# Kernel optimization log

Measured on AMD Instinct MI355X. Metric: run time of the kernel, lower is better.

Reference implementation:

```python
import jax, jax.numpy as jnp
import numpy as np

EPS = 1e-5
NH, NP = 12, 4  # heads, points per level


def _ln(x, g, b):
    m = x.mean(-1, keepdims=True)
    v = x.var(-1, keepdims=True)
    return (x - m) / jnp.sqrt(v + EPS) * g + b


def _bilinear(v, g, H_, W_):
    # v: [B, nh, H_*W_, d] flattened feature map; g: [B, nh, Lq, np, 2] normalized locs in [0,1]
    # torch grid_sample(align_corners=False, padding='zeros') with grid = 2*loc-1 => pixel = loc*W - 0.5
    x = g[..., 0] * W_ - 0.5
    y = g[..., 1] * H_ - 0.5
    x0 = jnp.floor(x)
    y0 = jnp.floor(y)
    wx1 = x - x0
    wy1 = y - y0
    wx0 = 1.0 - wx1
    wy0 = 1.0 - wy1
    d = v.shape[-1]
    Bn, nh, Lq, np_ = x.shape
    out = jnp.zeros((Bn, nh, Lq, np_, d), v.dtype)
    for xi, yi, w in ((x0, y0, wx0 * wy0), (x0 + 1, y0, wx1 * wy0),
                      (x0, y0 + 1, wx0 * wy1), (x0 + 1, y0 + 1, wx1 * wy1)):
        valid = (xi >= 0) & (xi < W_) & (yi >= 0) & (yi < H_)
        xc = jnp.clip(xi, 0, W_ - 1).astype(jnp.int32)
        yc = jnp.clip(yi, 0, H_ - 1).astype(jnp.int32)
        idx = (yc * W_ + xc).reshape(Bn, nh, Lq * np_, 1)
        gv = jnp.take_along_axis(v, idx, axis=2).reshape(Bn, nh, Lq, np_, d)
        out = out + (w * valid.astype(v.dtype))[..., None] * gv
    return out


def setup_inputs() -> dict:
    key = jax.random.key(0)
    ks = jax.random.split(key, 16)
    B, Lq, C = 4, 4096, 768
    nl = 1
    Hs = Ws = 64
    Lin = Hs * Ws
    hid = int(C * 0.25)
    s = 0.02
    f32 = jnp.float32
    return {
        'query': jax.random.normal(ks[0], (B, Lq, C), f32),
        'reference_points': jax.random.uniform(ks[1], (B, Lq, nl, 2), f32),
        'feat': jax.random.normal(ks[2], (B, Lin, C), f32),
        'spatial_shapes': np.array([[Hs, Ws]], dtype=np.int64),
        'level_start_index': np.array([0], dtype=np.int64),
        'H': Hs, 'W': Ws,
        'qn_g': jnp.ones(C, f32), 'qn_b': jnp.zeros(C, f32),
        'fn_g': jnp.ones(C, f32), 'fn_b': jnp.zeros(C, f32),
        'Wv': jax.random.normal(ks[3], (C, C), f32) * s, 'bv': jnp.zeros(C, f32),
        'Woff': jax.random.normal(ks[4], (C, NH * nl * NP * 2), f32) * s,
        'boff': jax.random.normal(ks[5], (NH * nl * NP * 2,), f32) * 0.1,
        'Watt': jax.random.normal(ks[6], (C, NH * nl * NP), f32) * s,
        'batt': jnp.zeros(NH * nl * NP, f32),
        'Wout': jax.random.normal(ks[7], (C, C), f32) * s, 'bout': jnp.zeros(C, f32),
        'ffn_g': jnp.ones(C, f32), 'ffn_b': jnp.zeros(C, f32),
        'W1': jax.random.normal(ks[8], (C, hid), f32) * s, 'b1': jnp.zeros(hid, f32),
        'W2': jax.random.normal(ks[9], (hid, C), f32) * s, 'b2': jnp.zeros(C, f32),
    }


def reference(query, reference_points, feat, spatial_shapes, level_start_index, H, W,
              qn_g, qn_b, fn_g, fn_b, Wv, bv, Woff, boff, Watt, batt, Wout, bout,
              ffn_g, ffn_b, W1, b1, W2, b2):
    B, Lq, C = query.shape
    nl = spatial_shapes.shape[0]
    d = C // NH
    qn = _ln(query, qn_g, qn_b)
    fn = _ln(feat, fn_g, fn_b)
    value = (fn @ Wv + bv).reshape(B, -1, NH, d)
    off = (qn @ Woff + boff).reshape(B, Lq, NH, nl, NP, 2)
    attw = jax.nn.softmax((qn @ Watt + batt).reshape(B, Lq, NH, nl * NP), axis=-1)
    attw = attw.reshape(B, Lq, NH, nl, NP)
    # offset normalizer is [W_l, H_l]
    norm = np.stack([spatial_shapes[:, 1], spatial_shapes[:, 0]], -1).astype(np.float32)
    loc = reference_points[:, :, None, :, None, :] + off / jnp.asarray(norm)[None, None, None, :, None, :]
    out = jnp.zeros((B, NH, Lq, d), query.dtype)
    for l in range(nl):
        H_, W_ = int(spatial_shapes[l, 0]), int(spatial_shapes[l, 1])
        s0 = int(level_start_index[l])
        v = value[:, s0:s0 + H_ * W_].transpose(0, 2, 1, 3)       # [B, nh, HW, d]
        g = loc[:, :, :, l].transpose(0, 2, 1, 3, 4)              # [B, nh, Lq, np, 2]
        sampled = _bilinear(v, g, H_, W_)                         # [B, nh, Lq, np, d]
        w = attw[:, :, :, l].transpose(0, 2, 1, 3)                # [B, nh, Lq, np]
        out = out + jnp.sum(sampled * w[..., None], axis=3)
    attn = out.transpose(0, 2, 1, 3).reshape(B, Lq, C) @ Wout + bout
    query = query + attn
    h = _ln(query, ffn_g, ffn_b)
    h = jax.nn.gelu(h @ W1 + b1, approximate=False)
    return query + (h @ W2 + b2)
```

## Files before the change

### kernel.cpp

```cpp
#include <hip/hip_runtime.h>
#include <hip/hip_bf16.h>
#include <math.h>

#define B_    4
#define LQ    4096
#define CC    768
#define NH_   12
#define DH    64
#define NP_   4
#define HH    64
#define WW    64
#define HID   192
#define ROWS  (B_ * LQ)
#define EPS_  1e-5f

typedef __bf16 bf16x8 __attribute__((ext_vector_type(8)));
typedef __bf16 bf16x4 __attribute__((ext_vector_type(4)));
typedef float  f32x4  __attribute__((ext_vector_type(4)));

typedef __attribute__((address_space(3))) void* lds_vp;
typedef const __attribute__((address_space(1))) void* gbl_vp;

struct PrepJob { const float* W; __bf16* Wt; int K; int N; int Npad; };
struct PrepJobs { PrepJob j[6]; };

__inline__ __device__ float wave_sum64(float v) {
    #pragma unroll
    for (int o = 32; o > 0; o >>= 1) v += __shfl_down(v, o, 64);
    return v;
}

__global__ __launch_bounds__(256)
void ln2p_kernel(const float* __restrict__ x0, const float* __restrict__ g0,
                 const float* __restrict__ b0, __bf16* __restrict__ y0,
                 const float* __restrict__ x1, const float* __restrict__ g1,
                 const float* __restrict__ b1, __bf16* __restrict__ y1,
                 PrepJobs jobs) {
    __shared__ float tile[64][65];
    __shared__ float red[8];
    int bx = blockIdx.x;
    int t = threadIdx.x;

    if (bx >= 2 * ROWS) {
        int tid = bx - 2 * ROWS;
        PrepJob job = jobs.j[tid / 144];
        int rem = tid % 144;
        int k0 = (rem % 12) * 64, n0 = (rem / 12) * 64;
        if (k0 >= job.K || n0 >= job.Npad) return;
        int c = t & 63, r0 = t >> 6;
        #pragma unroll
        for (int i = 0; i < 16; ++i) {
            int kk = i * 4 + r0;
            float v = 0.f;
            if (k0 + kk < job.K && n0 + c < job.N) v = job.W[(size_t)(k0 + kk) * job.N + n0 + c];
            tile[kk][c] = v;
        }
        __syncthreads();
        #pragma unroll
        for (int i = 0; i < 16; ++i) {
            int nn = i * 4 + r0;
            if (n0 + nn < job.Npad && k0 + c < job.K)
                job.Wt[(size_t)(n0 + nn) * job.K + k0 + c] = (__bf16)tile[c][nn];
        }
        return;
    }

    int sel = bx >= ROWS;
    int row = bx - sel * ROWS;
    const float* x = sel ? x1 : x0;
    const float* g = sel ? g1 : g0;
    const float* b = sel ? b1 : b0;
    __bf16* y = sel ? y1 : y0;
    const float* xr = x + (size_t)row * CC;
    __bf16* yr = y + (size_t)row * CC;
    f32x4 xv = {0.f, 0.f, 0.f, 0.f};
    if (t < 192) xv = *(const f32x4*)(xr + t * 4);
    float s  = xv[0] + xv[1] + xv[2] + xv[3];
    float s2 = xv[0]*xv[0] + xv[1]*xv[1] + xv[2]*xv[2] + xv[3]*xv[3];
    float ws = wave_sum64(s), ws2 = wave_sum64(s2);
    int w = t >> 6;
    if ((t & 63) == 0) { red[w] = ws; red[4 + w] = ws2; }
    __syncthreads();
    float S  = red[0] + red[1] + red[2] + red[3];
    float S2 = red[4] + red[5] + red[6] + red[7];
    float mean = S / CC;
    float inv  = rsqrtf(S2 / CC - mean * mean + EPS_);
    if (t < 192) {
        f32x4 gv = *(const f32x4*)(g + t * 4);
        f32x4 bv = *(const f32x4*)(b + t * 4);
        bf16x4 o;
        #pragma unroll
        for (int e = 0; e < 4; ++e)
            o[e] = (__bf16)((xv[e] - mean) * inv * gv[e] + bv[e]);
        *(bf16x4*)(yr + t * 4) = o;
    }
}

__global__ __launch_bounds__(256)
void ln_bf_kernel(const __bf16* __restrict__ x, const float* __restrict__ g,
                  const float* __restrict__ b, __bf16* __restrict__ y) {
    int row = blockIdx.x;
    const __bf16* xr = x + (size_t)row * CC;
    __bf16* yr = y + (size_t)row * CC;
    int t = threadIdx.x;
    float xv[8]; bf16x8 raw = {};
    if (t < 96) raw = *(const bf16x8*)(xr + t * 8);
    float s = 0.f, s2 = 0.f;
    #pragma unroll
    for (int e = 0; e < 8; ++e) { xv[e] = (float)raw[e]; s += xv[e]; s2 += xv[e]*xv[e]; }
    __shared__ float red[8];
    float ws = wave_sum64(s), ws2 = wave_sum64(s2);
    int w = t >> 6;
    if ((t & 63) == 0) { red[w] = ws; red[4 + w] = ws2; }
    __syncthreads();
    float S  = red[0] + red[1] + red[2] + red[3];
    float S2 = red[4] + red[5] + red[6] + red[7];
    float mean = S / CC;
    float inv  = rsqrtf(S2 / CC - mean * mean + EPS_);
    if (t < 96) {
        bf16x8 o;
        #pragma unroll
        for (int e = 0; e < 8; ++e)
            o[e] = (__bf16)((xv[e] - mean) * inv * g[t * 8 + e] + b[t * 8 + e]);
        *(bf16x8*)(yr + t * 8) = o;
    }
}

struct G64Job {
    const __bf16* A; const __bf16* Bt;
    const float* ba; const float* bb;
    const void* res; void* out;
    int Nsplit, K, N, flags, nblk, gx;
};

__global__ __launch_bounds__(256, 8)
void gemm64g(G64Job j0, G64Job j1) {
    __shared__ __bf16 As[2][64 * 32];
    __shared__ __bf16 Bs[2][64 * 32];

    int bid = blockIdx.x;
    G64Job jb = j0;
    if (bid >= j0.nblk) { jb = j1; bid -= j0.nblk; }

    int t = threadIdx.x;
    int lane = t & 63, wave = t >> 6;

    int swz = (bid & 7) * (jb.nblk >> 3) + (bid >> 3);
    int bx = swz % jb.gx, by = swz / jb.gx;
    int bm = by * 64, bn = bx * 64;
    int K = jb.K, N = jb.N;

    f32x4 acc[4] = {};

    int row0 = t >> 2, kc0 = (t & 3) ^ ((row0 >> 1) & 3);
    const __bf16* a0 = jb.A  + (size_t)(bm + row0) * K + kc0 * 8;
    const __bf16* b0 = jb.Bt + (size_t)(bn + row0) * K + kc0 * 8;

    int rbase = wave * 16 + (lane & 15);
    int nbase = lane & 15;
    int kq = lane >> 4;

    #define STAGE(bi, kt) do {                                                                   \
        int koff_ = (kt) * 32;                                                                   \
        __builtin_amdgcn_global_load_lds((gbl_vp)(a0 + koff_), (lds_vp)&As[bi][t * 8], 16, 0, 0); \
        __builtin_amdgcn_global_load_lds((gbl_vp)(b0 + koff_), (lds_vp)&Bs[bi][t * 8], 16, 0, 0); \
    } while (0)

    #define COMPUTE(bi) do {                                                                     \
        bf16x8 afr = *(const bf16x8*)&As[bi][rbase * 32 + ((kq ^ ((rbase >> 1) & 3)) * 8)];      \
        _Pragma("unroll")                                                                        \
        for (int j = 0; j < 4; ++j) {                                                            \
            int n = nbase + j * 16;                                                              \
            bf16x8 bfr = *(const bf16x8*)&Bs[bi][n * 32 + ((kq ^ ((n >> 1) & 3)) * 8)];          \
            acc[j] = __builtin_amdgcn_mfma_f32_16x16x32_bf16(afr, bfr, acc[j], 0, 0, 0);         \
        }                                                                                        \
    } while (0)

    int nt = K >> 5;
    STAGE(0, 0);
    STAGE(1, 1);
    for (int tt = 0; tt < nt; ++tt) {
        int cur = tt & 1;
        if (tt < nt - 1) asm volatile("s_waitcnt vmcnt(2)\n\ts_barrier" ::: "memory");
        else             asm volatile("s_waitcnt vmcnt(0)\n\ts_barrier" ::: "memory");
        COMPUTE(cur);
        asm volatile("s_waitcnt lgkmcnt(0)\n\ts_barrier" ::: "memory");
        if (tt + 2 < nt) STAGE(cur, tt + 2);
    }

    #undef STAGE
    #undef COMPUTE

    int rowq = lane >> 4;
    int do_gelu = jb.flags & 1, out_bf = jb.flags & 2, res_bf = jb.flags & 4;
    const void* res = jb.res;
    #pragma unroll
    for (int j = 0; j < 4; ++j) {
        int c = bn + j * 16 + (lane & 15);
        if (c < N) {
            float bias = (c < jb.Nsplit) ? jb.ba[c] : jb.bb[c - jb.Nsplit];
            #pragma unroll
            for (int r = 0; r < 4; ++r) {
                int m = bm + wave * 16 + rowq * 4 + r;
                float v = acc[j][r] + bias;
                if (do_gelu) v = 0.5f * v * (1.f + erff(v * 0.70710678118f));
                size_t oi = (size_t)m * N + c;
                if (res) v += res_bf ? (float)((const __bf16*)res)[oi]
                                     : ((const float*)res)[oi];
                if (out_bf) ((__bf16*)jb.out)[oi] = (__bf16)v;
                else        ((float*)jb.out)[oi]  = v;
            }
        }
    }
}

__global__ __launch_bounds__(256)
void sample_kernel(const __bf16* __restrict__ value, const float* __restrict__ offatt,
                   const float* __restrict__ refp, __bf16* __restrict__ out) {
    int wid  = blockIdx.x * 4 + (threadIdx.x >> 6);
    int lane = threadIdx.x & 63;
    int h  = wid % NH_;
    int bq = wid / NH_;
    int b  = bq / LQ;

    const float* oa = offatt + (size_t)bq * 144;
    float rx = refp[(size_t)bq * 2 + 0] * (float)WW - 0.5f;
    float ry = refp[(size_t)bq * 2 + 1] * (float)HH - 0.5f;

    float l0 = oa[96 + h * 4 + 0], l1 = oa[96 + h * 4 + 1];
    float l2 = oa[96 + h * 4 + 2], l3 = oa[96 + h * 4 + 3];
    float mx = fmaxf(fmaxf(l0, l1), fmaxf(l2, l3));
    float e0 = __expf(l0 - mx), e1 = __expf(l1 - mx);
    float e2 = __expf(l2 - mx), e3 = __expf(l3 - mx);
    float rs = 1.f / (e0 + e1 + e2 + e3);

    int pp = lane >> 4;
    int g  = lane & 15;
    float wpl = (pp == 0) ? e0 : (pp == 1) ? e1 : (pp == 2) ? e2 : e3;
    wpl *= rs;

    const float* oxy = oa + h * 8 + pp * 2;
    float x = rx + oxy[0];
    float y = ry + oxy[1];
    float x0f = floorf(x), y0f = floorf(y);
    float wx1 = x - x0f, wy1 = y - y0f;
    float wx0 = 1.f - wx1, wy0 = 1.f - wy1;
    int x0 = (int)x0f, y0 = (int)y0f;
    int x1 = x0 + 1, y1 = y0 + 1;
    float mx0 = ((unsigned)x0 < (unsigned)WW) ? wx0 : 0.f;
    float mx1 = ((unsigned)x1 < (unsigned)WW) ? wx1 : 0.f;
    float my0 = (((unsigned)y0 < (unsigned)HH) ? wy0 : 0.f) * wpl;
    float my1 = (((unsigned)y1 < (unsigned)HH) ? wy1 : 0.f) * wpl;
    int xc0 = x0 & (WW - 1), xc1 = x1 & (WW - 1);
    int r0 = (y0 & (HH - 1)) << 6, r1 = (y1 & (HH - 1)) << 6;

    const __bf16* vbase = value + (size_t)b * (LQ * CC) + h * DH + g * 4;
    bf16x4 v00 = *(const bf16x4*)(vbase + (size_t)(r0 + xc0) * CC);
    bf16x4 v01 = *(const bf16x4*)(vbase + (size_t)(r0 + xc1) * CC);
    bf16x4 v10 = *(const bf16x4*)(vbase + (size_t)(r1 + xc0) * CC);
    bf16x4 v11 = *(const bf16x4*)(vbase + (size_t)(r1 + xc1) * CC);
    float w00 = mx0 * my0, w01 = mx1 * my0, w10 = mx0 * my1, w11 = mx1 * my1;

    f32x4 acc;
    #pragma unroll
    for (int e = 0; e < 4; ++e)
        acc[e] = w00 * (float)v00[e] + w01 * (float)v01[e]
               + w10 * (float)v10[e] + w11 * (float)v11[e];

    #pragma unroll
    for (int e = 0; e < 4; ++e) {
        acc[e] += __shfl_xor(acc[e], 16, 64);
        acc[e] += __shfl_xor(acc[e], 32, 64);
    }
    if (pp == 0) {
        bf16x4 o;
        o[0] = (__bf16)acc[0]; o[1] = (__bf16)acc[1];
        o[2] = (__bf16)acc[2]; o[3] = (__bf16)acc[3];
        *(bf16x4*)(out + (size_t)bq * CC + h * DH + g * 4) = o;
    }
}

extern "C" void kernel_launch(void* const* d_in, const int* in_sizes, int n_in,
                              void* d_out, int out_size, void* d_ws, size_t ws_size,
                              hipStream_t stream) {
    const float* query = (const float*)d_in[0];
    const float* refp  = (const float*)d_in[1];
    const float* feat  = (const float*)d_in[2];
    const float* qn_g  = (const float*)d_in[7];
    const float* qn_b  = (const float*)d_in[8];
    const float* fn_g  = (const float*)d_in[9];
    const float* fn_b  = (const float*)d_in[10];
    const float* Wv    = (const float*)d_in[11];
    const float* bv    = (const float*)d_in[12];
    const float* Woff  = (const float*)d_in[13];
    const float* boff  = (const float*)d_in[14];
    const float* Watt  = (const float*)d_in[15];
    const float* batt  = (const float*)d_in[16];
    const float* Wout  = (const float*)d_in[17];
    const float* bout  = (const float*)d_in[18];
    const float* ffn_g = (const float*)d_in[19];
    const float* ffn_b = (const float*)d_in[20];
    const float* W1    = (const float*)d_in[21];
    const float* b1    = (const float*)d_in[22];
    const float* W2    = (const float*)d_in[23];
    const float* b2    = (const float*)d_in[24];
    float* out = (float*)d_out;

    char* ws = (char*)d_ws;
    __bf16* WvT    = (__bf16*)(ws + 0);
    __bf16* WcombT = (__bf16*)(ws + 1179648);
    __bf16* WoutT  = (__bf16*)(ws + 1572864);
    __bf16* W1T    = (__bf16*)(ws + 2752512);
    __bf16* W2T    = (__bf16*)(ws + 3145728);
    float*  offatt_f = (float*)(ws + 3670016);
    __bf16* h1_bf    = (__bf16*)offatt_f;
    __bf16* bufA     = (__bf16*)(ws + 13107200);
    __bf16* qn_bf    = bufA;
    __bf16* value_bf = bufA;
    __bf16* bufB     = (__bf16*)(ws + 38273024);
    __bf16* fn_bf    = bufB;
    __bf16* samp_bf  = bufB;
    __bf16* h_bf     = bufB;
    __bf16* attn_bf  = (__bf16*)(ws + 63438848);

    dim3 blk(256);

    PrepJobs jobs;
    jobs.j[0] = {Wv,   WvT,             768, 768, 768};
    jobs.j[1] = {Woff, WcombT,          768,  96,  96};
    jobs.j[2] = {Watt, WcombT + 96*768, 768,  48,  96};
    jobs.j[3] = {Wout, WoutT,           768, 768, 768};
    jobs.j[4] = {W1,   W1T,             768, 192, 192};
    jobs.j[5] = {W2,   W2T,             192, 768, 768};
    ln2p_kernel<<<2 * ROWS + 864, blk, 0, stream>>>(query, qn_g, qn_b, qn_bf,
                                                    feat,  fn_g, fn_b, fn_bf, jobs);

    G64Job joff = {qn_bf, WcombT, boff, batt, nullptr, offatt_f,
                   96, CC, 144, 0, 768, 3};
    G64Job jval = {fn_bf, WvT, bv, bv, nullptr, value_bf,
                   CC, CC, CC, 2, 3072, 12};
    gemm64g<<<768 + 3072, blk, 0, stream>>>(joff, jval);

    sample_kernel<<<ROWS * NH_ / 4, blk, 0, stream>>>(value_bf, offatt_f, refp, samp_bf);

    G64Job jout = {samp_bf, WoutT, bout, bout, query, attn_bf,
                   CC, CC, CC, 2, 3072, 12};
    gemm64g<<<3072, blk, 0, stream>>>(jout, jout);

    ln_bf_kernel<<<ROWS, blk, 0, stream>>>(attn_bf, ffn_g, ffn_b, h_bf);

    G64Job jw1 = {h_bf, W1T, b1, b1, nullptr, h1_bf,
                  HID, CC, HID, 1 | 2, 768, 3};
    gemm64g<<<768, blk, 0, stream>>>(jw1, jw1);

    G64Job jw2 = {h1_bf, W2T, b2, b2, attn_bf, out,
                  CC, HID, CC, 4, 3072, 12};
    gemm64g<<<3072, blk, 0, stream>>>(jw2, jw2);
}
```

Baseline: 427.2 us.

## Switch all GEMM operands to FP8 with scaled weights and triple-buffered staging

```diff
diff --git a/kernel.cpp b/kernel.cpp
--- a/kernel.cpp
+++ b/kernel.cpp
@@ -21,7 +21,19 @@
 typedef __attribute__((address_space(3))) void* lds_vp;
 typedef const __attribute__((address_space(1))) void* gbl_vp;
 
-struct PrepJob { const float* W; __bf16* Wt; int K; int N; int Npad; };
+__device__ __forceinline__ unsigned pk4_f8(float a, float b, float c, float d) {
+    unsigned lo, hi;
+    asm volatile("v_cvt_pk_fp8_f32 %0, %1, %2" : "=v"(lo) : "v"(a), "v"(b));
+    asm volatile("v_cvt_pk_fp8_f32 %0, %1, %2" : "=v"(hi) : "v"(c), "v"(d));
+    return (lo & 0xffffu) | (hi << 16);
+}
+__device__ __forceinline__ unsigned char to_f8(float a) {
+    unsigned r;
+    asm volatile("v_cvt_pk_fp8_f32 %0, %1, %1" : "=v"(r) : "v"(a));
+    return (unsigned char)r;
+}
+
+struct PrepJob { const float* W; unsigned char* Wt; int K; int N; int Npad; };
 struct PrepJobs { PrepJob j[6]; };
 
 __inline__ __device__ float wave_sum64(float v) {
@@ -32,9 +44,9 @@
 
 __global__ __launch_bounds__(256)
 void ln2p_kernel(const float* __restrict__ x0, const float* __restrict__ g0,
-                 const float* __restrict__ b0, __bf16* __restrict__ y0,
+                 const float* __restrict__ b0, unsigned char* __restrict__ y0,
                  const float* __restrict__ x1, const float* __restrict__ g1,
-                 const float* __restrict__ b1, __bf16* __restrict__ y1,
+                 const float* __restrict__ b1, unsigned char* __restrict__ y1,
                  PrepJobs jobs) {
     __shared__ float tile[64][65];
     __shared__ float red[8];
@@ -60,7 +72,7 @@
         for (int i = 0; i < 16; ++i) {
             int nn = i * 4 + r0;
             if (n0 + nn < job.Npad && k0 + c < job.K)
-                job.Wt[(size_t)(n0 + nn) * job.K + k0 + c] = (__bf16)tile[c][nn];
+                job.Wt[(size_t)(n0 + nn) * job.K + k0 + c] = to_f8(tile[c][nn] * 64.f);
         }
         return;
     }
@@ -70,9 +82,9 @@
     const float* x = sel ? x1 : x0;
     const float* g = sel ? g1 : g0;
     const float* b = sel ? b1 : b0;
-    __bf16* y = sel ? y1 : y0;
+    unsigned char* y = sel ? y1 : y0;
     const float* xr = x + (size_t)row * CC;
-    __bf16* yr = y + (size_t)row * CC;
+    unsigned char* yr = y + (size_t)row * CC;
     f32x4 xv = {0.f, 0.f, 0.f, 0.f};
     if (t < 192) xv = *(const f32x4*)(xr + t * 4);
     float s  = xv[0] + xv[1] + xv[2] + xv[3];
@@ -88,20 +100,20 @@
     if (t < 192) {
         f32x4 gv = *(const f32x4*)(g + t * 4);
         f32x4 bv = *(const f32x4*)(b + t * 4);
-        bf16x4 o;
+        float o[4];
         #pragma unroll
         for (int e = 0; e < 4; ++e)
-            o[e] = (__bf16)((xv[e] - mean) * inv * gv[e] + bv[e]);
-        *(bf16x4*)(yr + t * 4) = o;
+            o[e] = (xv[e] - mean) * inv * gv[e] + bv[e];
+        *(unsigned*)(yr + t * 4) = pk4_f8(o[0], o[1], o[2], o[3]);
     }
 }
 
 __global__ __launch_bounds__(256)
 void ln_bf_kernel(const __bf16* __restrict__ x, const float* __restrict__ g,
-                  const float* __restrict__ b, __bf16* __restrict__ y) {
+                  const float* __restrict__ b, unsigned char* __restrict__ y) {
     int row = blockIdx.x;
     const __bf16* xr = x + (size_t)row * CC;
-    __bf16* yr = y + (size_t)row * CC;
+    unsigned char* yr = y + (size_t)row * CC;
     int t = threadIdx.x;
     float xv[8]; bf16x8 raw = {};
     if (t < 96) raw = *(const bf16x8*)(xr + t * 8);
@@ -118,25 +130,28 @@
     float mean = S / CC;
     float inv  = rsqrtf(S2 / CC - mean * mean + EPS_);
     if (t < 96) {
-        bf16x8 o;
+        float o[8];
         #pragma unroll
         for (int e = 0; e < 8; ++e)
-            o[e] = (__bf16)((xv[e] - mean) * inv * g[t * 8 + e] + b[t * 8 + e]);
-        *(bf16x8*)(yr + t * 8) = o;
+            o[e] = (xv[e] - mean) * inv * g[t * 8 + e] + b[t * 8 + e];
+        uint2 pk;
+        pk.x = pk4_f8(o[0], o[1], o[2], o[3]);
+        pk.y = pk4_f8(o[4], o[5], o[6], o[7]);
+        *(uint2*)(yr + t * 8) = pk;
     }
 }
 
 struct G64Job {
-    const __bf16* A; const __bf16* Bt;
+    const unsigned char* A; const unsigned char* Bt;
     const float* ba; const float* bb;
     const void* res; void* out;
     int Nsplit, K, N, flags, nblk, gx;
 };
 
 __global__ __launch_bounds__(256, 8)
-void gemm64g(G64Job j0, G64Job j1) {
-    __shared__ __bf16 As[2][64 * 32];
-    __shared__ __bf16 Bs[2][64 * 32];
+void gemm64f8(G64Job j0, G64Job j1) {
+    __shared__ unsigned char As[3][2048];
+    __shared__ unsigned char Bs[3][2048];
 
     int bid = blockIdx.x;
     G64Job jb = j0;
@@ -152,63 +167,78 @@
 
     f32x4 acc[4] = {};
 
-    int row0 = t >> 2, kc0 = (t & 3) ^ ((row0 >> 1) & 3);
-    const __bf16* a0 = jb.A  + (size_t)(bm + row0) * K + kc0 * 8;
-    const __bf16* b0 = jb.Bt + (size_t)(bn + row0) * K + kc0 * 8;
-
-    int rbase = wave * 16 + (lane & 15);
-    int nbase = lane & 15;
-    int kq = lane >> 4;
-
-    #define STAGE(bi, kt) do {                                                                   \
-        int koff_ = (kt) * 32;                                                                   \
-        __builtin_amdgcn_global_load_lds((gbl_vp)(a0 + koff_), (lds_vp)&As[bi][t * 8], 16, 0, 0); \
-        __builtin_amdgcn_global_load_lds((gbl_vp)(b0 + koff_), (lds_vp)&Bs[bi][t * 8], 16, 0, 0); \
+    int local = t & 127;
+    int r = local >> 1, hch = local & 1;
+    int sw = (r >> 2) & 1;
+    const unsigned char* sbase = (wave < 2)
+        ? jb.A  + (size_t)(bm + r) * K + ((hch ^ sw) << 4)
+        : jb.Bt + (size_t)(bn + r) * K + ((hch ^ sw) << 4);
+
+    int rsel = lane & 15, kq = lane >> 4;
+    int ra = wave * 16 + rsel;
+    int aoff = ra * 32 + ((((kq >> 1) ^ ((ra >> 2) & 1)) << 4) | ((kq & 1) << 3));
+    int boffs[4];
+    #pragma unroll
+    for (int j = 0; j < 4; ++j) {
+        int n = rsel + j * 16;
+        boffs[j] = n * 32 + ((((kq >> 1) ^ ((n >> 2) & 1)) << 4) | ((kq & 1) << 3));
+    }
+
+    #define STAGE(bi, kt) do {                                                                    \
+        if (wave < 2)                                                                             \
+            __builtin_amdgcn_global_load_lds((gbl_vp)(sbase + (kt) * 32),                         \
+                (lds_vp)&As[bi][t * 16], 16, 0, 0);                                               \
+        else                                                                                      \
+            __builtin_amdgcn_global_load_lds((gbl_vp)(sbase + (kt) * 32),                         \
+                (lds_vp)&Bs[bi][(t - 128) * 16], 16, 0, 0);                                       \
     } while (0)
 
-    #define COMPUTE(bi) do {                                                                     \
-        bf16x8 afr = *(const bf16x8*)&As[bi][rbase * 32 + ((kq ^ ((rbase >> 1) & 3)) * 8)];      \
-        _Pragma("unroll")                                                                        \
-        for (int j = 0; j < 4; ++j) {                                                            \
-            int n = nbase + j * 16;                                                              \
-            bf16x8 bfr = *(const bf16x8*)&Bs[bi][n * 32 + ((kq ^ ((n >> 1) & 3)) * 8)];          \
-            acc[j] = __builtin_amdgcn_mfma_f32_16x16x32_bf16(afr, bfr, acc[j], 0, 0, 0);         \
-        }                                                                                        \
+    #define COMPUTE(bi) do {                                                                      \
+        long afr = *(const long*)&As[bi][aoff];                                                   \
+        _Pragma("unroll")                                                                         \
+        for (int j = 0; j < 4; ++j) {                                                             \
+            long bfr = *(const long*)&Bs[bi][boffs[j]];                                           \
+            acc[j] = __builtin_amdgcn_mfma_f32_16x16x32_fp8_fp8(afr, bfr, acc[j], 0, 0, 0);       \
+        }                                                                                         \
     } while (0)
 
     int nt = K >> 5;
     STAGE(0, 0);
     STAGE(1, 1);
+    STAGE(2, 2);
+    int bi = 0;
     for (int tt = 0; tt < nt; ++tt) {
-        int cur = tt & 1;
-        if (tt < nt - 1) asm volatile("s_waitcnt vmcnt(2)\n\ts_barrier" ::: "memory");
-        else             asm volatile("s_waitcnt vmcnt(0)\n\ts_barrier" ::: "memory");
-        COMPUTE(cur);
+        if (tt < nt - 2)       asm volatile("s_waitcnt vmcnt(2)\n\ts_barrier" ::: "memory");
+        else if (tt == nt - 2) asm volatile("s_waitcnt vmcnt(1)\n\ts_barrier" ::: "memory");
+        else                   asm volatile("s_waitcnt vmcnt(0)\n\ts_barrier" ::: "memory");
+        COMPUTE(bi);
         asm volatile("s_waitcnt lgkmcnt(0)\n\ts_barrier" ::: "memory");
-        if (tt + 2 < nt) STAGE(cur, tt + 2);
+        if (tt + 3 < nt) STAGE(bi, tt + 3);
+        ++bi; if (bi == 3) bi = 0;
     }
 
     #undef STAGE
     #undef COMPUTE
 
     int rowq = lane >> 4;
-    int do_gelu = jb.flags & 1, out_bf = jb.flags & 2, res_bf = jb.flags & 4;
+    int do_gelu = jb.flags & 1, out_bf = jb.flags & 2, res_bf = jb.flags & 4, out_f8 = jb.flags & 8;
     const void* res = jb.res;
     #pragma unroll
     for (int j = 0; j < 4; ++j) {
-        int c = bn + j * 16 + (lane & 15);
+        int c = bn + j * 16 + rsel;
         if (c < N) {
             float bias = (c < jb.Nsplit) ? jb.ba[c] : jb.bb[c - jb.Nsplit];
             #pragma unroll
-            for (int r = 0; r < 4; ++r) {
-                int m = bm + wave * 16 + rowq * 4 + r;
-                float v = acc[j][r] + bias;
+            for (int r4 = 0; r4 < 4; ++r4) {
+                int m = bm + wave * 16 + rowq * 4 + r4;
+                float v = acc[j][r4] * 0.015625f + bias;
                 if (do_gelu) v = 0.5f * v * (1.f + erff(v * 0.70710678118f));
                 size_t oi = (size_t)m * N + c;
                 if (res) v += res_bf ? (float)((const __bf16*)res)[oi]
                                      : ((const float*)res)[oi];
-                if (out_bf) ((__bf16*)jb.out)[oi] = (__bf16)v;
-                else        ((float*)jb.out)[oi]  = v;
+                if (out_f8)      ((unsigned char*)jb.out)[oi] = to_f8(v);
+                else if (out_bf) ((__bf16*)jb.out)[oi] = (__bf16)v;
+                else             ((float*)jb.out)[oi]  = v;
             }
         }
     }
@@ -216,7 +246,7 @@
 
 __global__ __launch_bounds__(256)
 void sample_kernel(const __bf16* __restrict__ value, const float* __restrict__ offatt,
-                   const float* __restrict__ refp, __bf16* __restrict__ out) {
+                   const float* __restrict__ refp, unsigned char* __restrict__ out) {
     int wid  = blockIdx.x * 4 + (threadIdx.x >> 6);
     int lane = threadIdx.x & 63;
     int h  = wid % NH_;
@@ -273,10 +303,8 @@
         acc[e] += __shfl_xor(acc[e], 32, 64);
     }
     if (pp == 0) {
-        bf16x4 o;
-        o[0] = (__bf16)acc[0]; o[1] = (__bf16)acc[1];
-        o[2] = (__bf16)acc[2]; o[3] = (__bf16)acc[3];
-        *(bf16x4*)(out + (size_t)bq * CC + h * DH + g * 4) = o;
+        *(unsigned*)(out + (size_t)bq * CC + h * DH + g * 4) =
+            pk4_f8(acc[0], acc[1], acc[2], acc[3]);
     }
 }
 
@@ -307,53 +335,51 @@
     float* out = (float*)d_out;
 
     char* ws = (char*)d_ws;
-    __bf16* WvT    = (__bf16*)(ws + 0);
-    __bf16* WcombT = (__bf16*)(ws + 1179648);
-    __bf16* WoutT  = (__bf16*)(ws + 1572864);
-    __bf16* W1T    = (__bf16*)(ws + 2752512);
-    __bf16* W2T    = (__bf16*)(ws + 3145728);
+    unsigned char* Wv8    = (unsigned char*)(ws + 0);
+    unsigned char* Wcomb8 = (unsigned char*)(ws + 1179648);
+    unsigned char* Wout8  = (unsigned char*)(ws + 1572864);
+    unsigned char* W18    = (unsigned char*)(ws + 2752512);
+    unsigned char* W28    = (unsigned char*)(ws + 3145728);
     float*  offatt_f = (float*)(ws + 3670016);
-    __bf16* h1_bf    = (__bf16*)offatt_f;
-    __bf16* bufA     = (__bf16*)(ws + 13107200);
-    __bf16* qn_bf    = bufA;
-    __bf16* value_bf = bufA;
-    __bf16* bufB     = (__bf16*)(ws + 38273024);
-    __bf16* fn_bf    = bufB;
-    __bf16* samp_bf  = bufB;
-    __bf16* h_bf     = bufB;
+    unsigned char* h1_f8 = (unsigned char*)offatt_f;
+    __bf16* value_bf = (__bf16*)(ws + 13107200);
+    unsigned char* fn_f8   = (unsigned char*)(ws + 38273024);
+    unsigned char* samp_f8 = fn_f8;
+    unsigned char* qn_f8   = (unsigned char*)(ws + 50855936);
+    unsigned char* h_f8    = qn_f8;
     __bf16* attn_bf  = (__bf16*)(ws + 63438848);
 
     dim3 blk(256);
 
     PrepJobs jobs;
-    jobs.j[0] = {Wv,   WvT,             768, 768, 768};
-    jobs.j[1] = {Woff, WcombT,          768,  96,  96};
-    jobs.j[2] = {Watt, WcombT + 96*768, 768,  48,  96};
-    jobs.j[3] = {Wout, WoutT,           768, 768, 768};
-    jobs.j[4] = {W1,   W1T,             768, 192, 192};
-    jobs.j[5] = {W2,   W2T,             192, 768, 768};
-    ln2p_kernel<<<2 * ROWS + 864, blk, 0, stream>>>(query, qn_g, qn_b, qn_bf,
-                                                    feat,  fn_g, fn_b, fn_bf, jobs);
-
-    G64Job joff = {qn_bf, WcombT, boff, batt, nullptr, offatt_f,
+    jobs.j[0] = {Wv,   Wv8,             768, 768, 768};
+    jobs.j[1] = {Woff, Wcomb8,          768,  96,  96};
+    jobs.j[2] = {Watt, Wcomb8 + 96*768, 768,  48,  96};
+    jobs.j[3] = {Wout, Wout8,           768, 768, 768};
+    jobs.j[4] = {W1,   W18,             768, 192, 192};
+    jobs.j[5] = {W2,   W28,             192, 768, 768};
+    ln2p_kernel<<<2 * ROWS + 864, blk, 0, stream>>>(query, qn_g, qn_b, qn_f8,
+                                                    feat,  fn_g, fn_b, fn_f8, jobs);
+
+    G64Job joff = {qn_f8, Wcomb8, boff, batt, nullptr, offatt_f,
                    96, CC, 144, 0, 768, 3};
-    G64Job jval = {fn_bf, WvT, bv, bv, nullptr, value_bf,
+    G64Job jval = {fn_f8, Wv8, bv, bv, nullptr, value_bf,
                    CC, CC, CC, 2, 3072, 12};
-    gemm64g<<<768 + 3072, blk, 0, stream>>>(joff, jval);
-
-    sample_kernel<<<ROWS * NH_ / 4, blk, 0, stream>>>(value_bf, offatt_f, refp, samp_bf);
-
-    G64Job jout = {samp_bf, WoutT, bout, bout, query, attn_bf,
-                   CC, CC, CC, 2, 3072, 12};
-    gemm64g<<<3072, blk, 0, stream>>>(jout, jout);
-
-    ln_bf_kernel<<<ROWS, blk, 0, stream>>>(attn_bf, ffn_g, ffn_b, h_bf);
-
-    G64Job jw1 = {h_bf, W1T, b1, b1, nullptr, h1_bf,
-                  HID, CC, HID, 1 | 2, 768, 3};
-    gemm64g<<<768, blk, 0, stream>>>(jw1, jw1);
-
-    G64Job jw2 = {h1_bf, W2T, b2, b2, attn_bf, out,
+    gemm64f8<<<768 + 3072, blk, 0, stream>>>(joff, jval);
+
+    sample_kernel<<<ROWS * NH_ / 4, blk, 0, stream>>>(value_bf, offatt_f, refp, samp_f8);
+
+    G64Job jout5 = {samp_f8, Wout8, bout, bout, query, attn_bf,
+                    CC, CC, CC, 2, 3072, 12};
+    gemm64f8<<<3072, blk, 0, stream>>>(jout5, jout5);
+
+    ln_bf_kernel<<<ROWS, blk, 0, stream>>>(attn_bf, ffn_g, ffn_b, h_f8);
+
+    G64Job jw1 = {h_f8, W18, b1, b1, nullptr, h1_f8,
+                  HID, CC, HID, 1 | 8, 768, 3};
+    gemm64f8<<<768, blk, 0, stream>>>(jw1, jw1);
+
+    G64Job jw2 = {h1_f8, W28, b2, b2, attn_bf, out,
                   CC, HID, CC, 4, 3072, 12};
-    gemm64g<<<3072, blk, 0, stream>>>(jw2, jw2);
-}
+    gemm64f8<<<3072, blk, 0, stream>>>(jw2, jw2);
+}
```

Result: faster. 408.5 us (-4.4%).
